# Kernel tuning notes

Measured on AMD Instinct MI355X. Metric: run time of the kernel, lower is better.

Reference implementation:

```python
import jax, jax.numpy as jnp
import numpy as np
import math

N, E, R = 50000, 800000, 32
DIN = 128
H, D = 8, 16          # num_heads, head_dim; H*D == out_ent_feats == 128
HOP = 5
ALPHA = 0.1
EPS = 1e-5


def layer_norm(x, g, b):
    m = jnp.mean(x, axis=-1, keepdims=True)
    v = jnp.mean((x - m) ** 2, axis=-1, keepdims=True)
    return (x - m) * jax.lax.rsqrt(v + EPS) * g + b


def segment_softmax(e, dst, num_nodes):
    # e: [E, H] scores, softmax over incoming edges of each dst node
    m = jax.ops.segment_max(e, dst, num_segments=num_nodes)      # [N, H]
    ex = jnp.exp(e - m[dst])
    s = jax.ops.segment_sum(ex, dst, num_segments=num_nodes)     # [N, H]
    return ex / s[dst]


def setup_inputs() -> dict:
    key = jax.random.key(0)
    ks = jax.random.split(key, 12)
    gain = 0.02  # small init scale (small_init_gain-style)
    ent_feat = jax.random.normal(ks[0], (N, DIN), dtype=jnp.float32)
    rel_feat = jax.random.normal(ks[1], (R, DIN), dtype=jnp.float32)
    src = jax.random.randint(ks[2], (E,), 0, N, dtype=jnp.int32)
    # guarantee every node has in-degree >= 1 (DGL raises otherwise)
    dst_rand = jax.random.randint(ks[3], (E - N,), 0, N, dtype=jnp.int32)
    dst = jnp.concatenate([jnp.arange(N, dtype=jnp.int32), dst_rand])
    rid = jax.random.randint(ks[4], (E,), 0, R, dtype=jnp.int32)
    W_head = jax.random.normal(ks[5], (DIN, H * D), dtype=jnp.float32) * gain
    W_tail = jax.random.normal(ks[6], (DIN, H * D), dtype=jnp.float32) * gain
    W_ent = jax.random.normal(ks[7], (DIN, H * D), dtype=jnp.float32) * gain
    W_rel = jax.random.normal(ks[8], (DIN, H * D), dtype=jnp.float32) * gain
    attn_r = jax.random.normal(ks[9], (1, H, D), dtype=jnp.float32) * gain
    W1 = jax.random.normal(ks[10], (H * D, 4 * H * D), dtype=jnp.float32) * gain
    W2 = jax.random.normal(ks[11], (4 * H * D, H * D), dtype=jnp.float32) * gain
    return dict(
        ent_feat=ent_feat, rel_feat=rel_feat, src=src, dst=dst, rid=rid,
        W_head=W_head, W_tail=W_tail, W_ent=W_ent, W_rel=W_rel, attn_r=attn_r,
        ln_ent_g=jnp.ones((DIN,), jnp.float32), ln_ent_b=jnp.zeros((DIN,), jnp.float32),
        ln_rel_g=jnp.ones((DIN,), jnp.float32), ln_rel_b=jnp.zeros((DIN,), jnp.float32),
        ff_ln_g=jnp.ones((H * D,), jnp.float32), ff_ln_b=jnp.zeros((H * D,), jnp.float32),
        W1=W1, b1=jnp.zeros((4 * H * D,), jnp.float32),
        W2=W2, b2=jnp.zeros((H * D,), jnp.float32),
    )


def _forward(ent_feat, rel_feat, src, dst, rid,
             W_head, W_tail, W_ent, W_rel, attn_r,
             ln_ent_g, ln_ent_b, ln_rel_g, ln_rel_b, ff_ln_g, ff_ln_b,
             W1, b1, W2, b2):
    n = ent_feat.shape[0]
    x = layer_norm(ent_feat, ln_ent_g, ln_ent_b)
    feat_head = (x @ W_head).reshape(n, H, D)
    feat_tail = (x @ W_tail).reshape(n, H, D)
    feat_ent = (x @ W_ent).reshape(n, H, D)

    # per-edge dot-product attention score: u_dot_v('eh','et')
    e = jnp.sum(feat_head[src] * feat_tail[dst], axis=-1)          # [E, H]

    r = layer_norm(rel_feat, ln_rel_g, ln_rel_b)
    feat_rel = (r @ W_rel).reshape(R, H, D)
    er = jnp.sum(feat_rel * attn_r, axis=-1)                       # [R, H]
    e = e * er[rid]                                                # [E, H]

    # e_mul_v with log_in = log(in_degree) of dst node
    deg = jax.ops.segment_sum(jnp.ones((e.shape[0],), e.dtype), dst, num_segments=n)
    log_in = jnp.log(jnp.maximum(deg, 1.0))                        # [N]
    e = e * log_in[dst][:, None] / math.sqrt(D)

    a = segment_softmax(e, dst, n)                                 # [E, H]

    # PPR diffusion: feat <- (1-alpha) * A^T feat + alpha * feat_0
    feat = feat_ent
    for _ in range(HOP):
        msg = feat[src] * a[:, :, None]                            # [E, H, D]
        agg = jax.ops.segment_sum(msg, dst, num_segments=n)        # [N, H, D]
        feat = (1.0 - ALPHA) * agg + ALPHA * feat_ent

    # residual (Identity: in_ent_feats == out_ent_feats)
    rst = feat + ent_feat.reshape(n, H, D)
    rst = rst.reshape(n, H * D)

    h = layer_norm(rst, ff_ln_g, ff_ln_b)
    ff = jax.nn.relu(h @ W1 + b1) @ W2 + b2
    return ff + rst


def reference(ent_feat, rel_feat, src, dst, rid,
              W_head, W_tail, W_ent, W_rel, attn_r,
              ln_ent_g, ln_ent_b, ln_rel_g, ln_rel_b, ff_ln_g, ff_ln_b,
              W1, b1, W2, b2):
    return _forward(ent_feat, rel_feat, src, dst, rid,
                    W_head, W_tail, W_ent, W_rel, attn_r,
                    ln_ent_g, ln_ent_b, ln_rel_g, ln_rel_b, ff_ln_g, ff_ln_b,
                    W1, b1, W2, b2)
```

## Files before the change

kernel.cpp:

```cpp
#include <hip/hip_runtime.h>
#include <hip/hip_bf16.h>

#define N_NODES 50000
#define N_EDGES 800000
#define N_REL 32
#define DIN 128
#define NH 8
#define HD 16
#define FF_HID 512
#define EPS_LN 1e-5f

typedef __attribute__((ext_vector_type(8))) short bf16x8;
typedef __attribute__((ext_vector_type(4))) float f32x4;
typedef __attribute__((ext_vector_type(2))) float f32x2;
typedef unsigned short ushort_t;
typedef unsigned int uint_t;

static __device__ __forceinline__ unsigned short f2bf(float f) {
    union { float f; unsigned u; } v; v.f = f;
    unsigned r = (v.u + 0x7fffu + ((v.u >> 16) & 1u)) >> 16;
    return (unsigned short)r;
}
static __device__ __forceinline__ float bf2f(unsigned u16) {
    union { unsigned u; float f; } v; v.u = u16 << 16; return v.f;
}
static __device__ __forceinline__ unsigned char f2fp8(float f) {
    return (unsigned char)(__builtin_amdgcn_cvt_pk_fp8_f32(f, f, 0, false) & 0xff);
}

__global__ void hist_kernel(const int* __restrict__ dst, int* __restrict__ deg, int E) {
    int i = blockIdx.x * blockDim.x + threadIdx.x;
    int stride = gridDim.x * blockDim.x;
    for (; i < E; i += stride) atomicAdd(&deg[dst[i]], 1);
}

__global__ __launch_bounds__(1024) void scan2_kernel(const int* __restrict__ deg,
                                                     int* __restrict__ row_off, int n) {
    __shared__ int lds[1024];
    __shared__ int wsum[16];
    __shared__ int s_base;
    int b = blockIdx.x, tid = threadIdx.x;
    int start = b * 1024;
    int partial = 0;
    for (int i = tid; i < start; i += 1024) partial += deg[i];
    for (int m = 32; m > 0; m >>= 1) partial += __shfl_down(partial, m);
    int wid = tid >> 6, lane = tid & 63;
    if (lane == 0) wsum[wid] = partial;
    __syncthreads();
    if (tid == 0) {
        int s = 0;
#pragma unroll
        for (int w = 0; w < 16; w++) s += wsum[w];
        s_base = s;
    }
    int i = start + tid;
    int v = (i < n) ? deg[i] : 0;
    lds[tid] = v;
    __syncthreads();
    for (int off = 1; off < 1024; off <<= 1) {
        int t = (tid >= off) ? lds[tid - off] : 0;
        __syncthreads();
        lds[tid] += t;
        __syncthreads();
    }
    int base = s_base;
    if (i < n) row_off[i] = base + lds[tid] - v;
    if (i == n - 1) row_off[n] = base + lds[tid];
}

__global__ void scatter_kernel(const int* __restrict__ src, const int* __restrict__ dst,
                               const int* __restrict__ rid, const int* __restrict__ row_off,
                               int* __restrict__ cursor, int* __restrict__ sr_perm, int E) {
    int i = blockIdx.x * blockDim.x + threadIdx.x;
    int stride = gridDim.x * blockDim.x;
    for (; i < E; i += stride) {
        int u = dst[i];
        int p = row_off[u] + atomicAdd(&cursor[u], 1);
        sr_perm[p] = src[i] | (rid[i] << 16);
    }
}

__global__ void pack_w_kernel(const float* __restrict__ W, short* __restrict__ out,
                              int K, int Ncols) {
    int idx = blockIdx.x * blockDim.x + threadIdx.x;
    int KT = K >> 5;
    int total = KT * (Ncols >> 4) * 64;
    if (idx >= total) return;
    int l = idx & 63;
    int tile = idx >> 6;
    int kt = tile & (KT - 1);
    int ct = tile / KT;
    int c = ct * 16 + (l & 15);
    int k0 = kt * 32 + ((l >> 4) * 8);
    bf16x8 v;
#pragma unroll
    for (int j = 0; j < 8; j++) v[j] = (short)f2bf(W[(size_t)(k0 + j) * Ncols + c]);
    *(bf16x8*)(out + (size_t)idx * 8) = v;
}

__global__ __launch_bounds__(128) void rel_kernel(const float* __restrict__ rel_feat,
                                                  const float* __restrict__ g,
                                                  const float* __restrict__ b,
                                                  const float* __restrict__ W_rel,
                                                  const float* __restrict__ attn_r,
                                                  float* __restrict__ er) {
    __shared__ float red[128];
    __shared__ float xs[128];
    __shared__ float prod[128];
    int r = blockIdx.x, tid = threadIdx.x;
    float x = rel_feat[r * DIN + tid];
    red[tid] = x;
    __syncthreads();
    for (int off = 64; off > 0; off >>= 1) {
        if (tid < off) red[tid] += red[tid + off];
        __syncthreads();
    }
    float mean = red[0] * (1.f / DIN);
    __syncthreads();
    red[tid] = x * x;
    __syncthreads();
    for (int off = 64; off > 0; off >>= 1) {
        if (tid < off) red[tid] += red[tid + off];
        __syncthreads();
    }
    float var = red[0] * (1.f / DIN) - mean * mean;
    float rs = rsqrtf(var + EPS_LN);
    xs[tid] = (x - mean) * rs * g[tid] + b[tid];
    __syncthreads();
    float acc = 0.f;
    for (int k = 0; k < DIN; k++) acc += xs[k] * W_rel[k * DIN + tid];
    prod[tid] = acc * attn_r[tid];
    __syncthreads();
    if (tid < NH) {
        float s = 0.f;
        for (int d = 0; d < HD; d++) s += prod[tid * HD + d];
        er[r * NH + tid] = s;
    }
}

__global__ __launch_bounds__(256) void proj_mfma_kernel(
    const float* __restrict__ ent, const float* __restrict__ g, const float* __restrict__ b,
    const short* __restrict__ Whp, const short* __restrict__ Wtp,
    const short* __restrict__ Wep, unsigned char* __restrict__ head_fp8,
    ushort_t* __restrict__ tail_bf, ushort_t* __restrict__ entp_bf) {
    __shared__ float xs[32][128];
    __shared__ short hsb[32][136];
    int tid = threadIdx.x;
    int base = blockIdx.x * 32;
    {
        int c = tid & 127, rb = tid >> 7;
#pragma unroll
        for (int j = 0; j < 16; j++) {
            int r = j * 2 + rb;
            int row = base + r;
            xs[r][c] = (row < N_NODES) ? ent[(size_t)row * DIN + c] : 0.f;
        }
    }
    __syncthreads();
    int wave = tid >> 6, lane = tid & 63;
    {
        float g0 = g[lane], g1 = g[lane + 64], bb0 = b[lane], bb1 = b[lane + 64];
        for (int r = wave * 8; r < wave * 8 + 8; r++) {
            float x0 = xs[r][lane], x1 = xs[r][lane + 64];
            float s1 = x0 + x1, s2 = x0 * x0 + x1 * x1;
            for (int m = 1; m < 64; m <<= 1) {
                s1 += __shfl_xor(s1, m);
                s2 += __shfl_xor(s2, m);
            }
            float mean = s1 * (1.f / DIN);
            float var = s2 * (1.f / DIN) - mean * mean;
            float rs = rsqrtf(var + EPS_LN);
            hsb[r][lane] = (short)f2bf((x0 - mean) * rs * g0 + bb0);
            hsb[r][lane + 64] = (short)f2bf((x1 - mean) * rs * g1 + bb1);
        }
    }
    __syncthreads();
    bf16x8 a[2][4];
#pragma unroll
    for (int rt = 0; rt < 2; rt++)
#pragma unroll
        for (int kt = 0; kt < 4; kt++)
            a[rt][kt] = *(const bf16x8*)&hsb[rt * 16 + (lane & 15)][kt * 32 + (lane >> 4) * 8];
#pragma unroll
    for (int m = 0; m < 3; m++) {
        const bf16x8* bp = (m == 0)   ? (const bf16x8*)Whp
                           : (m == 1) ? (const bf16x8*)Wtp
                                      : (const bf16x8*)Wep;
#pragma unroll
        for (int c2 = 0; c2 < 2; c2++) {
            int ct = wave * 2 + c2;
            f32x4 acc0 = {0.f, 0.f, 0.f, 0.f}, acc1 = {0.f, 0.f, 0.f, 0.f};
#pragma unroll
            for (int kt = 0; kt < 4; kt++) {
                bf16x8 bf = bp[(ct * 4 + kt) * 64 + lane];
                acc0 = __builtin_amdgcn_mfma_f32_16x16x32_bf16(a[0][kt], bf, acc0, 0, 0, 0);
                acc1 = __builtin_amdgcn_mfma_f32_16x16x32_bf16(a[1][kt], bf, acc1, 0, 0, 0);
            }
            int col = ct * 16 + (lane & 15);
            int r0 = (lane >> 4) * 4;
#pragma unroll
            for (int j = 0; j < 4; j++) {
                int row0 = base + r0 + j, row1 = base + 16 + r0 + j;
                if (m == 0) {
                    if (row0 < N_NODES) head_fp8[(size_t)row0 * DIN + col] = f2fp8(acc0[j]);
                    if (row1 < N_NODES) head_fp8[(size_t)row1 * DIN + col] = f2fp8(acc1[j]);
                } else if (m == 1) {
                    if (row0 < N_NODES) tail_bf[(size_t)row0 * DIN + col] = f2bf(acc0[j]);
                    if (row1 < N_NODES) tail_bf[(size_t)row1 * DIN + col] = f2bf(acc1[j]);
                } else {
                    if (row0 < N_NODES) entp_bf[(size_t)row0 * DIN + col] = f2bf(acc0[j]);
                    if (row1 < N_NODES) entp_bf[(size_t)row1 * DIN + col] = f2bf(acc1[j]);
                }
            }
        }
    }
}

__global__ __launch_bounds__(256) void scores_kernel(
    const unsigned char* __restrict__ head_fp8, const ushort_t* __restrict__ tail_bf,
    const float* __restrict__ er, const int* __restrict__ row_off,
    const int* __restrict__ sr_perm, ushort_t* __restrict__ a_bf,
    float* __restrict__ inv9) {
    int wid = threadIdx.x >> 6;
    int u = blockIdx.x * 4 + wid;
    int lane = threadIdx.x & 63;
    int h = lane & 7, esub = lane >> 3;
    int p0 = row_off[u], p1 = row_off[u + 1];
    int deg = p1 - p0;
    float scale = logf((float)(deg > 0 ? deg : 1)) * 0.25f;
    float t[16];
    {
        const uint_t* tp = (const uint_t*)(tail_bf + (size_t)u * DIN + h * HD);
#pragma unroll
        for (int i = 0; i < 8; i++) {
            uint_t w = tp[i];
            t[2 * i] = bf2f(w & 0xffffu);
            t[2 * i + 1] = bf2f(w >> 16);
        }
    }
    float ssum = 0.f;
    for (int p = p0 + esub; p < p1; p += 8) {
        int v = sr_perm[p];
        int s = v & 0xffff;
        int rr = v >> 16;
        const uint_t* hp = (const uint_t*)(head_fp8 + (size_t)s * DIN + h * HD);
        float dot = 0.f;
#pragma unroll
        for (int i = 0; i < 4; i++) {
            uint_t w = hp[i];
            f32x2 lo = __builtin_amdgcn_cvt_pk_f32_fp8(w, false);
            f32x2 hi = __builtin_amdgcn_cvt_pk_f32_fp8(w, true);
            dot += lo.x * t[4 * i] + lo.y * t[4 * i + 1] + hi.x * t[4 * i + 2] +
                   hi.y * t[4 * i + 3];
        }
        float e = dot * er[rr * NH + h] * scale;
        float sx = expf(e);
        a_bf[(size_t)p * NH + h] = f2bf(sx);
        ssum += sx;
    }
    ssum += __shfl_xor(ssum, 8);
    ssum += __shfl_xor(ssum, 16);
    ssum += __shfl_xor(ssum, 32);
    if (lane < 8) inv9[(size_t)u * NH + lane] = 0.9f / ssum;
}

__global__ __launch_bounds__(256) void diffuse_kernel(const ushort_t* __restrict__ fin,
                                                      const ushort_t* __restrict__ entp_bf,
                                                      const ushort_t* __restrict__ a_bf,
                                                      const int* __restrict__ sr_perm,
                                                      const int* __restrict__ row_off,
                                                      const float* __restrict__ inv9,
                                                      ushort_t* __restrict__ fout) {
    int wid = threadIdx.x >> 6;
    int u = blockIdx.x * 4 + wid;
    int lane = threadIdx.x & 63;
    int hh = lane >> 3;
    int p0 = row_off[u], p1 = row_off[u + 1];
    float acc0 = 0.f, acc1 = 0.f;
    int p = p0;
    for (; p + 4 <= p1; p += 4) {
        int s0 = sr_perm[p] & 0xffff, s1 = sr_perm[p + 1] & 0xffff;
        int s2 = sr_perm[p + 2] & 0xffff, s3 = sr_perm[p + 3] & 0xffff;
        float a0 = bf2f(a_bf[(size_t)p * NH + hh]);
        float a1 = bf2f(a_bf[(size_t)(p + 1) * NH + hh]);
        float a2 = bf2f(a_bf[(size_t)(p + 2) * NH + hh]);
        float a3 = bf2f(a_bf[(size_t)(p + 3) * NH + hh]);
        uint_t v0 = *(const uint_t*)(fin + (size_t)s0 * DIN + 2 * lane);
        uint_t v1 = *(const uint_t*)(fin + (size_t)s1 * DIN + 2 * lane);
        uint_t v2 = *(const uint_t*)(fin + (size_t)s2 * DIN + 2 * lane);
        uint_t v3 = *(const uint_t*)(fin + (size_t)s3 * DIN + 2 * lane);
        acc0 += a0 * bf2f(v0 & 0xffffu) + a1 * bf2f(v1 & 0xffffu) +
                a2 * bf2f(v2 & 0xffffu) + a3 * bf2f(v3 & 0xffffu);
        acc1 += a0 * bf2f(v0 >> 16) + a1 * bf2f(v1 >> 16) + a2 * bf2f(v2 >> 16) +
                a3 * bf2f(v3 >> 16);
    }
    for (; p < p1; ++p) {
        int s0 = sr_perm[p] & 0xffff;
        float a0 = bf2f(a_bf[(size_t)p * NH + hh]);
        uint_t v0 = *(const uint_t*)(fin + (size_t)s0 * DIN + 2 * lane);
        acc0 += a0 * bf2f(v0 & 0xffffu);
        acc1 += a0 * bf2f(v0 >> 16);
    }
    float iv = inv9[(size_t)u * NH + hh];
    size_t o = (size_t)u * DIN + 2 * lane;
    uint_t e = *(const uint_t*)(entp_bf + o);
    float x0 = iv * acc0 + 0.1f * bf2f(e & 0xffffu);
    float x1 = iv * acc1 + 0.1f * bf2f(e >> 16);
    *(uint_t*)(fout + o) = (uint_t)f2bf(x0) | ((uint_t)f2bf(x1) << 16);
}

static __device__ __forceinline__ int hid_idx(int row, int col) {
    return row * 512 + ((((col >> 3) & 63) ^ (row & 7)) << 3) + (col & 7);
}
__global__ __launch_bounds__(256) void ffn_mfma_kernel(
    const ushort_t* __restrict__ feat, const float* __restrict__ ent0,
    const float* __restrict__ g, const float* __restrict__ b,
    const short* __restrict__ W1p, const float* __restrict__ b1,
    const short* __restrict__ W2p, const float* __restrict__ b2,
    float* __restrict__ out) {
    __shared__ ushort_t rst_bf[32][136];
    __shared__ short hs[32][136];
    __shared__ short hid[32 * 512];
    int tid = threadIdx.x;
    int base = blockIdx.x * 32;
    int wave = tid >> 6, lane = tid & 63;
    {
        int c = tid & 127, rb = tid >> 7;
        float g_c = g[c], b_c = b[c];
        (void)g_c; (void)b_c;
#pragma unroll
        for (int j = 0; j < 16; j++) {
            int r = j * 2 + rb;
            int row = base + r;
            float v = 0.f;
            if (row < N_NODES) {
                size_t idx = (size_t)row * DIN + c;
                v = bf2f(feat[idx]) + ent0[idx];
            }
            rst_bf[r][c] = f2bf(v);
        }
    }
    __syncthreads();
    {
        float g0 = g[lane], g1 = g[lane + 64], bb0 = b[lane], bb1 = b[lane + 64];
        for (int r = wave * 8; r < wave * 8 + 8; r++) {
            float x0 = bf2f(rst_bf[r][lane]), x1 = bf2f(rst_bf[r][lane + 64]);
            float s1 = x0 + x1, s2 = x0 * x0 + x1 * x1;
            for (int m = 1; m < 64; m <<= 1) {
                s1 += __shfl_xor(s1, m);
                s2 += __shfl_xor(s2, m);
            }
            float mean = s1 * (1.f / DIN);
            float var = s2 * (1.f / DIN) - mean * mean;
            float rs = rsqrtf(var + EPS_LN);
            hs[r][lane] = (short)f2bf((x0 - mean) * rs * g0 + bb0);
            hs[r][lane + 64] = (short)f2bf((x1 - mean) * rs * g1 + bb1);
        }
    }
    __syncthreads();
    {
        bf16x8 a[2][4];
#pragma unroll
        for (int rt = 0; rt < 2; rt++)
#pragma unroll
            for (int kt = 0; kt < 4; kt++)
                a[rt][kt] =
                    *(const bf16x8*)&hs[rt * 16 + (lane & 15)][kt * 32 + (lane >> 4) * 8];
        const bf16x8* bp = (const bf16x8*)W1p;
        for (int cti = 0; cti < 8; cti++) {
            int ct = wave * 8 + cti;
            f32x4 acc0 = {0.f, 0.f, 0.f, 0.f}, acc1 = {0.f, 0.f, 0.f, 0.f};
#pragma unroll
            for (int kt = 0; kt < 4; kt++) {
                bf16x8 bf = bp[(ct * 4 + kt) * 64 + lane];
                acc0 = __builtin_amdgcn_mfma_f32_16x16x32_bf16(a[0][kt], bf, acc0, 0, 0, 0);
                acc1 = __builtin_amdgcn_mfma_f32_16x16x32_bf16(a[1][kt], bf, acc1, 0, 0, 0);
            }
            int col = ct * 16 + (lane & 15);
            float bv = b1[col];
            int r0 = (lane >> 4) * 4;
#pragma unroll
            for (int j = 0; j < 4; j++) {
                hid[hid_idx(r0 + j, col)] = (short)f2bf(fmaxf(acc0[j] + bv, 0.f));
                hid[hid_idx(16 + r0 + j, col)] = (short)f2bf(fmaxf(acc1[j] + bv, 0.f));
            }
        }
    }
    __syncthreads();
    {
        f32x4 acc[2][2] = {{{0.f, 0.f, 0.f, 0.f}, {0.f, 0.f, 0.f, 0.f}},
                           {{0.f, 0.f, 0.f, 0.f}, {0.f, 0.f, 0.f, 0.f}}};
        const bf16x8* bp2 = (const bf16x8*)W2p;
        for (int kt = 0; kt < 16; kt++) {
            int row0 = lane & 15, row1 = 16 + (lane & 15);
            int col8 = kt * 32 + (lane >> 4) * 8;
            bf16x8 a0 = *(const bf16x8*)&hid[hid_idx(row0, col8)];
            bf16x8 a1 = *(const bf16x8*)&hid[hid_idx(row1, col8)];
#pragma unroll
            for (int c2 = 0; c2 < 2; c2++) {
                int ct = wave * 2 + c2;
                bf16x8 bf = bp2[(ct * 16 + kt) * 64 + lane];
                acc[0][c2] = __builtin_amdgcn_mfma_f32_16x16x32_bf16(a0, bf, acc[0][c2], 0, 0, 0);
                acc[1][c2] = __builtin_amdgcn_mfma_f32_16x16x32_bf16(a1, bf, acc[1][c2], 0, 0, 0);
            }
        }
#pragma unroll
        for (int rt = 0; rt < 2; rt++)
#pragma unroll
            for (int c2 = 0; c2 < 2; c2++) {
                int col = (wave * 2 + c2) * 16 + (lane & 15);
                float bv = b2[col];
                int r0 = rt * 16 + (lane >> 4) * 4;
#pragma unroll
                for (int j = 0; j < 4; j++) {
                    int row = base + r0 + j;
                    if (row < N_NODES)
                        out[(size_t)row * DIN + col] =
                            acc[rt][c2][j] + bv + bf2f(rst_bf[r0 + j][col]);
                }
            }
    }
}

extern "C" void kernel_launch(void* const* d_in, const int* in_sizes, int n_in,
                              void* d_out, int out_size, void* d_ws, size_t ws_size,
                              hipStream_t stream) {
    const float* ent_feat = (const float*)d_in[0];
    const float* rel_feat = (const float*)d_in[1];
    const int* src = (const int*)d_in[2];
    const int* dst = (const int*)d_in[3];
    const int* rid = (const int*)d_in[4];
    const float* W_head = (const float*)d_in[5];
    const float* W_tail = (const float*)d_in[6];
    const float* W_ent = (const float*)d_in[7];
    const float* W_rel = (const float*)d_in[8];
    const float* attn_r = (const float*)d_in[9];
    const float* ln_ent_g = (const float*)d_in[10];
    const float* ln_ent_b = (const float*)d_in[11];
    const float* ln_rel_g = (const float*)d_in[12];
    const float* ln_rel_b = (const float*)d_in[13];
    const float* ff_ln_g = (const float*)d_in[14];
    const float* ff_ln_b = (const float*)d_in[15];
    const float* W1 = (const float*)d_in[16];
    const float* b1 = (const float*)d_in[17];
    const float* W2 = (const float*)d_in[18];
    const float* b2 = (const float*)d_in[19];
    float* out = (float*)d_out;

    const int N = N_NODES, E = N_EDGES;

    char* cur = (char*)d_ws;
    auto alloc = [&](size_t bytes, size_t align) -> void* {
        uintptr_t p = (uintptr_t)cur;
        p = (p + align - 1) & ~(uintptr_t)(align - 1);
        cur = (char*)(p + bytes);
        return (void*)p;
    };
    ushort_t* tail_bf = (ushort_t*)alloc((size_t)N * DIN * 2, 16);
    ushort_t* entp_bf = (ushort_t*)alloc((size_t)N * DIN * 2, 16);
    ushort_t* diffA = (ushort_t*)alloc((size_t)N * DIN * 2, 16);
    unsigned char* head_fp8 = (unsigned char*)alloc((size_t)N * DIN, 16);
    int* sr_perm = (int*)alloc((size_t)E * 4, 16);
    int* row_off = (int*)alloc((size_t)(N + 1) * 4, 16);
    int* deg = (int*)alloc((size_t)2 * N * 4, 16);
    int* cursor = deg + N;
    float* er = (float*)alloc((size_t)N_REL * NH * 4, 16);
    float* inv9 = (float*)alloc((size_t)N * NH * 4, 16);
    short* W1p = (short*)alloc((size_t)DIN * FF_HID * 2, 16);
    short* W2p = (short*)alloc((size_t)FF_HID * DIN * 2, 16);
    short* Whp = (short*)alloc((size_t)DIN * DIN * 2, 16);
    short* Wtp = (short*)alloc((size_t)DIN * DIN * 2, 16);
    short* Wep = (short*)alloc((size_t)DIN * DIN * 2, 16);
    ushort_t* a_fit = (ushort_t*)alloc((size_t)E * NH * 2, 16);
    ushort_t* a_bf = ((size_t)(cur - (char*)d_ws) <= ws_size) ? a_fit : (ushort_t*)d_out;

    hipMemsetAsync(deg, 0, sizeof(int) * 2 * (size_t)N, stream);
    pack_w_kernel<<<32, 256, 0, stream>>>(W1, W1p, DIN, FF_HID);
    pack_w_kernel<<<32, 256, 0, stream>>>(W2, W2p, FF_HID, DIN);
    pack_w_kernel<<<8, 256, 0, stream>>>(W_head, Whp, DIN, DIN);
    pack_w_kernel<<<8, 256, 0, stream>>>(W_tail, Wtp, DIN, DIN);
    pack_w_kernel<<<8, 256, 0, stream>>>(W_ent, Wep, DIN, DIN);

    hist_kernel<<<1024, 256, 0, stream>>>(dst, deg, E);
    scan2_kernel<<<(N + 1023) / 1024, 1024, 0, stream>>>(deg, row_off, N);
    scatter_kernel<<<1024, 256, 0, stream>>>(src, dst, rid, row_off, cursor, sr_perm, E);
    rel_kernel<<<N_REL, 128, 0, stream>>>(rel_feat, ln_rel_g, ln_rel_b, W_rel, attn_r, er);
    int nblk32 = (N + 31) / 32;
    proj_mfma_kernel<<<nblk32, 256, 0, stream>>>(ent_feat, ln_ent_g, ln_ent_b, Whp, Wtp,
                                                 Wep, head_fp8, tail_bf, entp_bf);
    scores_kernel<<<N / 4, 256, 0, stream>>>(head_fp8, tail_bf, er, row_off, sr_perm,
                                             a_bf, inv9);
    diffuse_kernel<<<N / 4, 256, 0, stream>>>(entp_bf, entp_bf, a_bf, sr_perm, row_off,
                                              inv9, diffA);
    diffuse_kernel<<<N / 4, 256, 0, stream>>>(diffA, entp_bf, a_bf, sr_perm, row_off,
                                              inv9, tail_bf);
    diffuse_kernel<<<N / 4, 256, 0, stream>>>(tail_bf, entp_bf, a_bf, sr_perm, row_off,
                                              inv9, diffA);
    diffuse_kernel<<<N / 4, 256, 0, stream>>>(diffA, entp_bf, a_bf, sr_perm, row_off,
                                              inv9, tail_bf);
    diffuse_kernel<<<N / 4, 256, 0, stream>>>(tail_bf, entp_bf, a_bf, sr_perm, row_off,
                                              inv9, diffA);
    ffn_mfma_kernel<<<nblk32, 256, 0, stream>>>(diffA, ent_feat, ff_ln_g, ff_ln_b, W1p,
                                                b1, W2p, b2, out);
}
```

Baseline: 406.4 us.

## Store diffusion features in FP8 and merge small setup kernels into combo launches

The PPR diffusion hops now gather neighbor features from FP8 buffers instead of BF16, which halves the bytes of random gather traffic per edge. Only the last hop writes BF16 for the FFN. The histogram, weight packing and relation-score kernels are merged into one launch, and the edge scatter is merged with the projection kernel, cutting launch count and letting independent work overlap. The cost is reduced precision in the intermediate diffusion features, which risks accuracy drift across five hops.

```diff
diff --git a/kernel.cpp b/kernel.cpp
--- a/kernel.cpp
+++ b/kernel.cpp
@@ -27,11 +27,89 @@
 static __device__ __forceinline__ unsigned char f2fp8(float f) {
     return (unsigned char)(__builtin_amdgcn_cvt_pk_fp8_f32(f, f, 0, false) & 0xff);
 }
-
-__global__ void hist_kernel(const int* __restrict__ dst, int* __restrict__ deg, int E) {
-    int i = blockIdx.x * blockDim.x + threadIdx.x;
-    int stride = gridDim.x * blockDim.x;
-    for (; i < E; i += stride) atomicAdd(&deg[dst[i]], 1);
+static __device__ __forceinline__ ushort_t f2fp8x2(float x0, float x1) {
+    return (ushort_t)(__builtin_amdgcn_cvt_pk_fp8_f32(x0, x1, 0, false) & 0xffff);
+}
+
+static __device__ __forceinline__ void pack_dev(const float* __restrict__ W,
+                                                short* __restrict__ out, int K, int Ncols,
+                                                int idx) {
+    int KT = K >> 5;
+    int l = idx & 63;
+    int tile = idx >> 6;
+    int kt = tile & (KT - 1);
+    int ct = tile / KT;
+    int c = ct * 16 + (l & 15);
+    int k0 = kt * 32 + ((l >> 4) * 8);
+    bf16x8 v;
+#pragma unroll
+    for (int j = 0; j < 8; j++) v[j] = (short)f2bf(W[(size_t)(k0 + j) * Ncols + c]);
+    *(bf16x8*)(out + (size_t)idx * 8) = v;
+}
+
+#define C0_HIST 512
+__global__ __launch_bounds__(256) void combo0_kernel(
+    const int* __restrict__ dst, int* __restrict__ deg, const float* __restrict__ W1,
+    short* __restrict__ W1p, const float* __restrict__ W2, short* __restrict__ W2p,
+    const float* __restrict__ Wh, short* __restrict__ Whp, const float* __restrict__ Wt,
+    short* __restrict__ Wtp, const float* __restrict__ We, short* __restrict__ Wep,
+    const float* __restrict__ rel_feat, const float* __restrict__ gr,
+    const float* __restrict__ br, const float* __restrict__ W_rel,
+    const float* __restrict__ attn_r, float* __restrict__ er) {
+    __shared__ float red[128];
+    __shared__ float xsr[128];
+    __shared__ float prod[128];
+    int b = blockIdx.x, tid = threadIdx.x;
+    if (b < C0_HIST) {
+        int i = b * 256 + tid;
+        int stride = C0_HIST * 256;
+        for (; i < N_EDGES; i += stride) atomicAdd(&deg[dst[i]], 1);
+    } else if (b < C0_HIST + 32) {
+        pack_dev(W1, W1p, DIN, FF_HID, (b - C0_HIST) * 256 + tid);
+    } else if (b < C0_HIST + 64) {
+        pack_dev(W2, W2p, FF_HID, DIN, (b - C0_HIST - 32) * 256 + tid);
+    } else if (b < C0_HIST + 72) {
+        pack_dev(Wh, Whp, DIN, DIN, (b - C0_HIST - 64) * 256 + tid);
+    } else if (b < C0_HIST + 80) {
+        pack_dev(Wt, Wtp, DIN, DIN, (b - C0_HIST - 72) * 256 + tid);
+    } else if (b < C0_HIST + 88) {
+        pack_dev(We, Wep, DIN, DIN, (b - C0_HIST - 80) * 256 + tid);
+    } else {
+        int r = b - (C0_HIST + 88);
+        float x = 0.f;
+        if (tid < 128) {
+            x = rel_feat[r * DIN + tid];
+            red[tid] = x;
+        }
+        __syncthreads();
+        for (int off = 64; off > 0; off >>= 1) {
+            if (tid < off) red[tid] += red[tid + off];
+            __syncthreads();
+        }
+        float mean = red[0] * (1.f / DIN);
+        __syncthreads();
+        if (tid < 128) red[tid] = x * x;
+        __syncthreads();
+        for (int off = 64; off > 0; off >>= 1) {
+            if (tid < off) red[tid] += red[tid + off];
+            __syncthreads();
+        }
+        float var = red[0] * (1.f / DIN) - mean * mean;
+        float rs = rsqrtf(var + EPS_LN);
+        if (tid < 128) xsr[tid] = (x - mean) * rs * gr[tid] + br[tid];
+        __syncthreads();
+        if (tid < 128) {
+            float acc = 0.f;
+            for (int k = 0; k < DIN; k++) acc += xsr[k] * W_rel[k * DIN + tid];
+            prod[tid] = acc * attn_r[tid];
+        }
+        __syncthreads();
+        if (tid < NH) {
+            float s = 0.f;
+            for (int d = 0; d < HD; d++) s += prod[tid * HD + d];
+            er[r * NH + tid] = s;
+        }
+    }
 }
 
 __global__ __launch_bounds__(1024) void scan2_kernel(const int* __restrict__ deg,
@@ -68,85 +146,29 @@
     if (i == n - 1) row_off[n] = base + lds[tid];
 }
 
-__global__ void scatter_kernel(const int* __restrict__ src, const int* __restrict__ dst,
-                               const int* __restrict__ rid, const int* __restrict__ row_off,
-                               int* __restrict__ cursor, int* __restrict__ sr_perm, int E) {
-    int i = blockIdx.x * blockDim.x + threadIdx.x;
-    int stride = gridDim.x * blockDim.x;
-    for (; i < E; i += stride) {
-        int u = dst[i];
-        int p = row_off[u] + atomicAdd(&cursor[u], 1);
-        sr_perm[p] = src[i] | (rid[i] << 16);
-    }
-}
-
-__global__ void pack_w_kernel(const float* __restrict__ W, short* __restrict__ out,
-                              int K, int Ncols) {
-    int idx = blockIdx.x * blockDim.x + threadIdx.x;
-    int KT = K >> 5;
-    int total = KT * (Ncols >> 4) * 64;
-    if (idx >= total) return;
-    int l = idx & 63;
-    int tile = idx >> 6;
-    int kt = tile & (KT - 1);
-    int ct = tile / KT;
-    int c = ct * 16 + (l & 15);
-    int k0 = kt * 32 + ((l >> 4) * 8);
-    bf16x8 v;
-#pragma unroll
-    for (int j = 0; j < 8; j++) v[j] = (short)f2bf(W[(size_t)(k0 + j) * Ncols + c]);
-    *(bf16x8*)(out + (size_t)idx * 8) = v;
-}
-
-__global__ __launch_bounds__(128) void rel_kernel(const float* __restrict__ rel_feat,
-                                                  const float* __restrict__ g,
-                                                  const float* __restrict__ b,
-                                                  const float* __restrict__ W_rel,
-                                                  const float* __restrict__ attn_r,
-                                                  float* __restrict__ er) {
-    __shared__ float red[128];
-    __shared__ float xs[128];
-    __shared__ float prod[128];
-    int r = blockIdx.x, tid = threadIdx.x;
-    float x = rel_feat[r * DIN + tid];
-    red[tid] = x;
-    __syncthreads();
-    for (int off = 64; off > 0; off >>= 1) {
-        if (tid < off) red[tid] += red[tid + off];
-        __syncthreads();
-    }
-    float mean = red[0] * (1.f / DIN);
-    __syncthreads();
-    red[tid] = x * x;
-    __syncthreads();
-    for (int off = 64; off > 0; off >>= 1) {
-        if (tid < off) red[tid] += red[tid + off];
-        __syncthreads();
-    }
-    float var = red[0] * (1.f / DIN) - mean * mean;
-    float rs = rsqrtf(var + EPS_LN);
-    xs[tid] = (x - mean) * rs * g[tid] + b[tid];
-    __syncthreads();
-    float acc = 0.f;
-    for (int k = 0; k < DIN; k++) acc += xs[k] * W_rel[k * DIN + tid];
-    prod[tid] = acc * attn_r[tid];
-    __syncthreads();
-    if (tid < NH) {
-        float s = 0.f;
-        for (int d = 0; d < HD; d++) s += prod[tid * HD + d];
-        er[r * NH + tid] = s;
-    }
-}
-
-__global__ __launch_bounds__(256) void proj_mfma_kernel(
+#define C1_SCAT 1024
+__global__ __launch_bounds__(256) void combo1_kernel(
+    const int* __restrict__ src, const int* __restrict__ dst, const int* __restrict__ rid,
+    const int* __restrict__ row_off, int* __restrict__ cursor, int* __restrict__ sr_perm,
     const float* __restrict__ ent, const float* __restrict__ g, const float* __restrict__ b,
     const short* __restrict__ Whp, const short* __restrict__ Wtp,
     const short* __restrict__ Wep, unsigned char* __restrict__ head_fp8,
-    ushort_t* __restrict__ tail_bf, ushort_t* __restrict__ entp_bf) {
+    ushort_t* __restrict__ tail_bf, ushort_t* __restrict__ entp_bf,
+    unsigned char* __restrict__ entp_fp8) {
     __shared__ float xs[32][128];
     __shared__ short hsb[32][136];
-    int tid = threadIdx.x;
-    int base = blockIdx.x * 32;
+    int blk = blockIdx.x, tid = threadIdx.x;
+    if (blk < C1_SCAT) {
+        int i = blk * 256 + tid;
+        int stride = C1_SCAT * 256;
+        for (; i < N_EDGES; i += stride) {
+            int u = dst[i];
+            int p = row_off[u] + atomicAdd(&cursor[u], 1);
+            sr_perm[p] = src[i] | (rid[i] << 16);
+        }
+        return;
+    }
+    int base = (blk - C1_SCAT) * 32;
     {
         int c = tid & 127, rb = tid >> 7;
 #pragma unroll
@@ -208,8 +230,14 @@
                     if (row0 < N_NODES) tail_bf[(size_t)row0 * DIN + col] = f2bf(acc0[j]);
                     if (row1 < N_NODES) tail_bf[(size_t)row1 * DIN + col] = f2bf(acc1[j]);
                 } else {
-                    if (row0 < N_NODES) entp_bf[(size_t)row0 * DIN + col] = f2bf(acc0[j]);
-                    if (row1 < N_NODES) entp_bf[(size_t)row1 * DIN + col] = f2bf(acc1[j]);
+                    if (row0 < N_NODES) {
+                        entp_bf[(size_t)row0 * DIN + col] = f2bf(acc0[j]);
+                        entp_fp8[(size_t)row0 * DIN + col] = f2fp8(acc0[j]);
+                    }
+                    if (row1 < N_NODES) {
+                        entp_bf[(size_t)row1 * DIN + col] = f2bf(acc1[j]);
+                        entp_fp8[(size_t)row1 * DIN + col] = f2fp8(acc1[j]);
+                    }
                 }
             }
         }
@@ -264,13 +292,12 @@
     if (lane < 8) inv9[(size_t)u * NH + lane] = 0.9f / ssum;
 }
 
-__global__ __launch_bounds__(256) void diffuse_kernel(const ushort_t* __restrict__ fin,
-                                                      const ushort_t* __restrict__ entp_bf,
-                                                      const ushort_t* __restrict__ a_bf,
-                                                      const int* __restrict__ sr_perm,
-                                                      const int* __restrict__ row_off,
-                                                      const float* __restrict__ inv9,
-                                                      ushort_t* __restrict__ fout) {
+template <bool OUT_BF>
+__global__ __launch_bounds__(256) void diffuse8_kernel(
+    const unsigned char* __restrict__ fin8, const ushort_t* __restrict__ entp_bf,
+    const ushort_t* __restrict__ a_bf, const int* __restrict__ sr_perm,
+    const int* __restrict__ row_off, const float* __restrict__ inv9,
+    void* __restrict__ fout) {
     int wid = threadIdx.x >> 6;
     int u = blockIdx.x * 4 + wid;
     int lane = threadIdx.x & 63;
@@ -285,28 +312,35 @@
         float a1 = bf2f(a_bf[(size_t)(p + 1) * NH + hh]);
         float a2 = bf2f(a_bf[(size_t)(p + 2) * NH + hh]);
         float a3 = bf2f(a_bf[(size_t)(p + 3) * NH + hh]);
-        uint_t v0 = *(const uint_t*)(fin + (size_t)s0 * DIN + 2 * lane);
-        uint_t v1 = *(const uint_t*)(fin + (size_t)s1 * DIN + 2 * lane);
-        uint_t v2 = *(const uint_t*)(fin + (size_t)s2 * DIN + 2 * lane);
-        uint_t v3 = *(const uint_t*)(fin + (size_t)s3 * DIN + 2 * lane);
-        acc0 += a0 * bf2f(v0 & 0xffffu) + a1 * bf2f(v1 & 0xffffu) +
-                a2 * bf2f(v2 & 0xffffu) + a3 * bf2f(v3 & 0xffffu);
-        acc1 += a0 * bf2f(v0 >> 16) + a1 * bf2f(v1 >> 16) + a2 * bf2f(v2 >> 16) +
-                a3 * bf2f(v3 >> 16);
+        uint_t w0 = *(const ushort_t*)(fin8 + (size_t)s0 * DIN + 2 * lane);
+        uint_t w1 = *(const ushort_t*)(fin8 + (size_t)s1 * DIN + 2 * lane);
+        uint_t w2 = *(const ushort_t*)(fin8 + (size_t)s2 * DIN + 2 * lane);
+        uint_t w3 = *(const ushort_t*)(fin8 + (size_t)s3 * DIN + 2 * lane);
+        f32x2 v0 = __builtin_amdgcn_cvt_pk_f32_fp8(w0, false);
+        f32x2 v1 = __builtin_amdgcn_cvt_pk_f32_fp8(w1, false);
+        f32x2 v2 = __builtin_amdgcn_cvt_pk_f32_fp8(w2, false);
+        f32x2 v3 = __builtin_amdgcn_cvt_pk_f32_fp8(w3, false);
+        acc0 += a0 * v0.x + a1 * v1.x + a2 * v2.x + a3 * v3.x;
+        acc1 += a0 * v0.y + a1 * v1.y + a2 * v2.y + a3 * v3.y;
     }
     for (; p < p1; ++p) {
         int s0 = sr_perm[p] & 0xffff;
         float a0 = bf2f(a_bf[(size_t)p * NH + hh]);
-        uint_t v0 = *(const uint_t*)(fin + (size_t)s0 * DIN + 2 * lane);
-        acc0 += a0 * bf2f(v0 & 0xffffu);
-        acc1 += a0 * bf2f(v0 >> 16);
+        uint_t w0 = *(const ushort_t*)(fin8 + (size_t)s0 * DIN + 2 * lane);
+        f32x2 v0 = __builtin_amdgcn_cvt_pk_f32_fp8(w0, false);
+        acc0 += a0 * v0.x;
+        acc1 += a0 * v0.y;
     }
     float iv = inv9[(size_t)u * NH + hh];
     size_t o = (size_t)u * DIN + 2 * lane;
     uint_t e = *(const uint_t*)(entp_bf + o);
     float x0 = iv * acc0 + 0.1f * bf2f(e & 0xffffu);
     float x1 = iv * acc1 + 0.1f * bf2f(e >> 16);
-    *(uint_t*)(fout + o) = (uint_t)f2bf(x0) | ((uint_t)f2bf(x1) << 16);
+    if (OUT_BF) {
+        *(uint_t*)((ushort_t*)fout + o) = (uint_t)f2bf(x0) | ((uint_t)f2bf(x1) << 16);
+    } else {
+        *(ushort_t*)((unsigned char*)fout + o) = f2fp8x2(x0, x1);
+    }
 }
 
 static __device__ __forceinline__ int hid_idx(int row, int col) {
@@ -326,8 +360,6 @@
     int wave = tid >> 6, lane = tid & 63;
     {
         int c = tid & 127, rb = tid >> 7;
-        float g_c = g[c], b_c = b[c];
-        (void)g_c; (void)b_c;
 #pragma unroll
         for (int j = 0; j < 16; j++) {
             int r = j * 2 + rb;
@@ -458,7 +490,9 @@
     };
     ushort_t* tail_bf = (ushort_t*)alloc((size_t)N * DIN * 2, 16);
     ushort_t* entp_bf = (ushort_t*)alloc((size_t)N * DIN * 2, 16);
-    ushort_t* diffA = (ushort_t*)alloc((size_t)N * DIN * 2, 16);
+    unsigned char* entp_fp8 = (unsigned char*)alloc((size_t)N * DIN, 16);
+    unsigned char* f8A = (unsigned char*)alloc((size_t)N * DIN, 16);
+    unsigned char* f8B = (unsigned char*)alloc((size_t)N * DIN, 16);
     unsigned char* head_fp8 = (unsigned char*)alloc((size_t)N * DIN, 16);
     int* sr_perm = (int*)alloc((size_t)E * 4, 16);
     int* row_off = (int*)alloc((size_t)(N + 1) * 4, 16);
@@ -475,31 +509,26 @@
     ushort_t* a_bf = ((size_t)(cur - (char*)d_ws) <= ws_size) ? a_fit : (ushort_t*)d_out;
 
     hipMemsetAsync(deg, 0, sizeof(int) * 2 * (size_t)N, stream);
-    pack_w_kernel<<<32, 256, 0, stream>>>(W1, W1p, DIN, FF_HID);
-    pack_w_kernel<<<32, 256, 0, stream>>>(W2, W2p, FF_HID, DIN);
-    pack_w_kernel<<<8, 256, 0, stream>>>(W_head, Whp, DIN, DIN);
-    pack_w_kernel<<<8, 256, 0, stream>>>(W_tail, Wtp, DIN, DIN);
-    pack_w_kernel<<<8, 256, 0, stream>>>(W_ent, Wep, DIN, DIN);
-
-    hist_kernel<<<1024, 256, 0, stream>>>(dst, deg, E);
+    combo0_kernel<<<632, 256, 0, stream>>>(dst, deg, W1, W1p, W2, W2p, W_head, Whp,
+                                           W_tail, Wtp, W_ent, Wep, rel_feat, ln_rel_g,
+                                           ln_rel_b, W_rel, attn_r, er);
     scan2_kernel<<<(N + 1023) / 1024, 1024, 0, stream>>>(deg, row_off, N);
-    scatter_kernel<<<1024, 256, 0, stream>>>(src, dst, rid, row_off, cursor, sr_perm, E);
-    rel_kernel<<<N_REL, 128, 0, stream>>>(rel_feat, ln_rel_g, ln_rel_b, W_rel, attn_r, er);
     int nblk32 = (N + 31) / 32;
-    proj_mfma_kernel<<<nblk32, 256, 0, stream>>>(ent_feat, ln_ent_g, ln_ent_b, Whp, Wtp,
-                                                 Wep, head_fp8, tail_bf, entp_bf);
+    combo1_kernel<<<C1_SCAT + nblk32, 256, 0, stream>>>(
+        src, dst, rid, row_off, cursor, sr_perm, ent_feat, ln_ent_g, ln_ent_b, Whp, Wtp,
+        Wep, head_fp8, tail_bf, entp_bf, entp_fp8);
     scores_kernel<<<N / 4, 256, 0, stream>>>(head_fp8, tail_bf, er, row_off, sr_perm,
                                              a_bf, inv9);
-    diffuse_kernel<<<N / 4, 256, 0, stream>>>(entp_bf, entp_bf, a_bf, sr_perm, row_off,
-                                              inv9, diffA);
-    diffuse_kernel<<<N / 4, 256, 0, stream>>>(diffA, entp_bf, a_bf, sr_perm, row_off,
-                                              inv9, tail_bf);
-    diffuse_kernel<<<N / 4, 256, 0, stream>>>(tail_bf, entp_bf, a_bf, sr_perm, row_off,
-                                              inv9, diffA);
-    diffuse_kernel<<<N / 4, 256, 0, stream>>>(diffA, entp_bf, a_bf, sr_perm, row_off,
-                                              inv9, tail_bf);
-    diffuse_kernel<<<N / 4, 256, 0, stream>>>(tail_bf, entp_bf, a_bf, sr_perm, row_off,
-                                              inv9, diffA);
-    ffn_mfma_kernel<<<nblk32, 256, 0, stream>>>(diffA, ent_feat, ff_ln_g, ff_ln_b, W1p,
+    diffuse8_kernel<false><<<N / 4, 256, 0, stream>>>(entp_fp8, entp_bf, a_bf, sr_perm,
+                                                      row_off, inv9, f8A);
+    diffuse8_kernel<false><<<N / 4, 256, 0, stream>>>(f8A, entp_bf, a_bf, sr_perm,
+                                                      row_off, inv9, f8B);
+    diffuse8_kernel<false><<<N / 4, 256, 0, stream>>>(f8B, entp_bf, a_bf, sr_perm,
+                                                      row_off, inv9, f8A);
+    diffuse8_kernel<false><<<N / 4, 256, 0, stream>>>(f8A, entp_bf, a_bf, sr_perm,
+                                                      row_off, inv9, f8B);
+    diffuse8_kernel<true><<<N / 4, 256, 0, stream>>>(f8B, entp_bf, a_bf, sr_perm,
+                                                     row_off, inv9, tail_bf);
+    ffn_mfma_kernel<<<nblk32, 256, 0, stream>>>(tail_bf, ent_feat, ff_ln_g, ff_ln_b, W1p,
                                                 b1, W2p, b2, out);
 }
```

Result: faster. 367.9 us (-9.5%).
